# Kernel tuning notes

Measured on AMD Instinct MI355X. Metric: run time of the kernel, lower is better.

Reference implementation:

```python
import jax, jax.numpy as jnp
import numpy as np


def _vieta_pell_basis(x, degree):
    # Iterative recurrence: V0 = 2, V1 = x, Vn = x*V_{n-1} + V_{n-2}
    basis = [2.0 * jnp.ones_like(x), x]
    for _ in range(2, degree + 1):
        basis.append(x * basis[-1] + basis[-2])
    return jnp.stack(basis[: degree + 1], axis=-1)  # [b, i, d+1]


def setup_inputs() -> dict:
    key = jax.random.key(0)
    k1, k2 = jax.random.split(key)
    batch, input_dim, output_dim, degree = 4096, 1024, 1024, 8
    x = jax.random.normal(k1, (batch, input_dim), dtype=jnp.float32)
    std = 1.0 / (input_dim * (degree + 1))
    vp_coeffs = jax.random.normal(k2, (input_dim, output_dim, degree + 1), dtype=jnp.float32) * std
    return {"x": x, "vp_coeffs": vp_coeffs}


def reference(x, vp_coeffs):
    degree = vp_coeffs.shape[-1] - 1
    xt = jnp.tanh(x)  # [b, i]
    vp_basis = _vieta_pell_basis(xt, degree)  # [b, i, d+1]
    y = jnp.einsum("bid,iod->bo", vp_basis, vp_coeffs)
    return y
```

## Files before the change

kernel.cpp:

```cpp
#include <hip/hip_runtime.h>
#include <hip/hip_bf16.h>

typedef unsigned short u16;
typedef unsigned int   u32;

#define BATCH 4096
#define IDIM  1024
#define ODIM  1024
#define NDEG  9
#define KTOT  (IDIM * NDEG)

#define BM 128
#define BN 128
#define BKK 64

typedef __attribute__((ext_vector_type(8))) short short8_t;
typedef __attribute__((ext_vector_type(4))) float f32x4;

__device__ __forceinline__ u16 f2bf(float f) {
    union { float f; u32 u; } v; v.f = f;
    u32 r = v.u + 0x7FFFu + ((v.u >> 16) & 1u);
    return (u16)(r >> 16);
}
__device__ __forceinline__ u32 pack2bf(float lo, float hi) {
    return (u32)f2bf(lo) | ((u32)f2bf(hi) << 16);
}

__device__ __forceinline__ void gl_lds16(const u16* g, u16* l) {
    __builtin_amdgcn_global_load_lds(
        (const __attribute__((address_space(1))) void*)g,
        (__attribute__((address_space(3))) void*)l,
        16, 0, 0);
}

__global__ void prep_a_kernel(const float* __restrict__ x, u16* __restrict__ A) {
    int t  = blockIdx.x * 256 + threadIdx.x;
    int b  = t >> 9;
    int i2 = (t & 511) << 1;
    float2 xv = ((const float2*)x)[t];
    float t0 = tanhf(xv.x), t1 = tanhf(xv.y);
    u32* dst = (u32*)(A + (size_t)b * KTOT + i2);
    float a0 = 2.0f, a1 = 2.0f;
    float b0 = t0,  b1 = t1;
    dst[0]   = pack2bf(2.0f, 2.0f);
    dst[512] = pack2bf(t0, t1);
#pragma unroll
    for (int d = 2; d < NDEG; ++d) {
        float n0 = t0 * b0 + a0;
        float n1 = t1 * b1 + a1;
        dst[(size_t)d * 512] = pack2bf(n0, n1);
        a0 = b0; b0 = n0; a1 = b1; b1 = n1;
    }
}

__global__ void prep_b_kernel(const float* __restrict__ c, u16* __restrict__ Bt) {
    int t = blockIdx.x * 256 + threadIdx.x;
    int o = t >> 10;
    int i = t & 1023;
    const float* src = c + ((size_t)i * ODIM + o) * NDEG;
    u16* dst = Bt + (size_t)o * KTOT + i;
#pragma unroll
    for (int d = 0; d < NDEG; ++d)
        dst[(size_t)d * 1024] = f2bf(src[d]);
}

__global__ __launch_bounds__(256, 2)
void gemm_kernel(const u16* __restrict__ A, const u16* __restrict__ B,
                 float* __restrict__ C, int kLen) {
    __shared__ __align__(16) u16 ldsA[BM * BKK];
    __shared__ __align__(16) u16 ldsB[BN * BKK];

    const int tid  = threadIdx.x;
    const int lane = tid & 63;
    const int wave = tid >> 6;
    const int quad = lane >> 4;
    const int l15  = lane & 15;
    const int wm   = wave & 1;
    const int wn   = wave >> 1;
    const int bm   = blockIdx.y;
    const int bn   = blockIdx.x;
    const int kStart = blockIdx.z * kLen;
    C += (size_t)blockIdx.z * BATCH * ODIM;

    const u16* ga[4]; const u16* gb[4];
    u16* la[4]; u16* lb[4];
#pragma unroll
    for (int t = 0; t < 4; ++t) {
        int s  = t * 256 + tid;
        int r  = s >> 3;
        int sc = (s & 7) ^ (r & 7);
        ga[t] = A + (size_t)(bm * BM + r) * KTOT + kStart + sc * 8;
        gb[t] = B + (size_t)(bn * BN + r) * KTOT + kStart + sc * 8;
        la[t] = ldsA + s * 8;
        lb[t] = ldsB + s * 8;
    }

    f32x4 acc[4][4];
#pragma unroll
    for (int mt = 0; mt < 4; ++mt)
#pragma unroll
        for (int nt = 0; nt < 4; ++nt)
            acc[mt][nt] = (f32x4){0.f, 0.f, 0.f, 0.f};

    const int nIter = kLen / BKK;
    for (int it = 0; it < nIter; ++it) {
#pragma unroll
        for (int t = 0; t < 4; ++t) gl_lds16(ga[t], la[t]);
#pragma unroll
        for (int t = 0; t < 4; ++t) gl_lds16(gb[t], lb[t]);
        __syncthreads();

#pragma unroll
        for (int kk = 0; kk < 2; ++kk) {
            short8_t af[4], bfg[4];
#pragma unroll
            for (int mt = 0; mt < 4; ++mt) {
                int row = wm * 64 + mt * 16 + l15;
                int pc  = (kk * 4 + quad) ^ (row & 7);
                af[mt] = *(const short8_t*)(ldsA + (row * 8 + pc) * 8);
            }
#pragma unroll
            for (int nt = 0; nt < 4; ++nt) {
                int row = wn * 64 + nt * 16 + l15;
                int pc  = (kk * 4 + quad) ^ (row & 7);
                bfg[nt] = *(const short8_t*)(ldsB + (row * 8 + pc) * 8);
            }
#pragma unroll
            for (int mt = 0; mt < 4; ++mt)
#pragma unroll
                for (int nt = 0; nt < 4; ++nt)
                    acc[mt][nt] = __builtin_amdgcn_mfma_f32_16x16x32_bf16(
                        af[mt], bfg[nt], acc[mt][nt], 0, 0, 0);
        }
        __syncthreads();

#pragma unroll
        for (int t = 0; t < 4; ++t) { ga[t] += BKK; gb[t] += BKK; }
    }

#pragma unroll
    for (int mt = 0; mt < 4; ++mt) {
#pragma unroll
        for (int nt = 0; nt < 4; ++nt) {
            int row0 = bm * BM + wm * 64 + mt * 16 + quad * 4;
            int col  = bn * BN + wn * 64 + nt * 16 + l15;
#pragma unroll
            for (int r = 0; r < 4; ++r)
                C[(size_t)(row0 + r) * ODIM + col] = acc[mt][nt][r];
        }
    }
}

__global__ void reduce_kernel(const float* __restrict__ P, float* __restrict__ out) {
    int t = blockIdx.x * 256 + threadIdx.x;
    f32x4 a = ((const f32x4*)P)[t];
    f32x4 b = ((const f32x4*)(P + (size_t)BATCH * ODIM))[t];
    ((f32x4*)out)[t] = a + b;
}

extern "C" void kernel_launch(void* const* d_in, const int* in_sizes, int n_in,
                              void* d_out, int out_size, void* d_ws, size_t ws_size,
                              hipStream_t stream) {
    const float* x      = (const float*)d_in[0];
    const float* coeffs = (const float*)d_in[1];
    float* out = (float*)d_out;

    u16* A  = (u16*)d_ws;
    u16* Bt = A + (size_t)BATCH * KTOT;
    float* P = (float*)(Bt + (size_t)ODIM * KTOT);

    size_t need_base  = ((size_t)BATCH * KTOT + (size_t)ODIM * KTOT) * 2;
    size_t need_split = need_base + (size_t)2 * BATCH * ODIM * 4;

    prep_a_kernel<<<BATCH * IDIM / 512, 256, 0, stream>>>(x, A);
    prep_b_kernel<<<ODIM * IDIM / 256, 256, 0, stream>>>(coeffs, Bt);

    if (ws_size >= need_split) {
        dim3 grid(ODIM / BN, BATCH / BM, 2);
        gemm_kernel<<<grid, 256, 0, stream>>>(A, Bt, P, KTOT / 2);
        reduce_kernel<<<BATCH * ODIM / 1024, 256, 0, stream>>>(P, out);
    } else {
        dim3 grid(ODIM / BN, BATCH / BM, 1);
        gemm_kernel<<<grid, 256, 0, stream>>>(A, Bt, out, KTOT);
    }
}
```

Before: 220.1 us.

## Transpose coefficients through LDS tiles and raise split-K to four partitions

The coefficient prep kernel now stages a 128x72 tile in shared memory, so global reads are contiguous and writes to the transposed bf16 matrix are 8-byte vectors, replacing strided scalar accesses. The GEMM split-K factor goes from 2 to 4 when workspace allows, which gives more blocks to fill the CUs, and launch bounds ask for 4 blocks per CU. The reduce kernel becomes generic over S. The cost is more partial-sum traffic and a larger reduce, and the higher occupancy hint may cause register spills.

```diff
diff --git a/kernel.cpp b/kernel.cpp
--- a/kernel.cpp
+++ b/kernel.cpp
@@ -3,6 +3,7 @@
 
 typedef unsigned short u16;
 typedef unsigned int   u32;
+typedef unsigned long long u64;
 
 #define BATCH 4096
 #define IDIM  1024
@@ -53,18 +54,41 @@
     }
 }
 
+#define PB_TI 128
+#define PB_TO 8
+#define PB_J  (PB_TO * NDEG)
+#define PB_LS 132
+
 __global__ void prep_b_kernel(const float* __restrict__ c, u16* __restrict__ Bt) {
-    int t = blockIdx.x * 256 + threadIdx.x;
-    int o = t >> 10;
-    int i = t & 1023;
-    const float* src = c + ((size_t)i * ODIM + o) * NDEG;
-    u16* dst = Bt + (size_t)o * KTOT + i;
-#pragma unroll
-    for (int d = 0; d < NDEG; ++d)
-        dst[(size_t)d * 1024] = f2bf(src[d]);
-}
-
-__global__ __launch_bounds__(256, 2)
+    __shared__ u16 lds[PB_J * PB_LS];
+    const int tid = threadIdx.x;
+    const int i0  = blockIdx.y * PB_TI;
+    const int o0  = blockIdx.x * PB_TO;
+    const float* src = c + (size_t)i0 * (ODIM * NDEG) + (size_t)o0 * NDEG;
+
+#pragma unroll
+    for (int t = 0; t < 36; ++t) {
+        int f  = t * 256 + tid;
+        int ii = f / PB_J;
+        int j  = f - ii * PB_J;
+        float v = src[(size_t)ii * (ODIM * NDEG) + j];
+        lds[j * PB_LS + ii] = f2bf(v);
+    }
+    __syncthreads();
+
+#pragma unroll
+    for (int t = 0; t < 9; ++t) {
+        int g   = t * 256 + tid;
+        int j   = g >> 5;
+        int ii4 = (g & 31) << 2;
+        int o   = j / NDEG;
+        int d   = j - o * NDEG;
+        u64 v = *(const u64*)(lds + j * PB_LS + ii4);
+        *(u64*)(Bt + (size_t)(o0 + o) * KTOT + d * 1024 + i0 + ii4) = v;
+    }
+}
+
+__global__ __launch_bounds__(256, 4)
 void gemm_kernel(const u16* __restrict__ A, const u16* __restrict__ B,
                  float* __restrict__ C, int kLen) {
     __shared__ __align__(16) u16 ldsA[BM * BKK];
@@ -151,11 +175,13 @@
     }
 }
 
-__global__ void reduce_kernel(const float* __restrict__ P, float* __restrict__ out) {
+__global__ void reduce_kernel(const float* __restrict__ P, float* __restrict__ out,
+                              int S) {
     int t = blockIdx.x * 256 + threadIdx.x;
     f32x4 a = ((const f32x4*)P)[t];
-    f32x4 b = ((const f32x4*)(P + (size_t)BATCH * ODIM))[t];
-    ((f32x4*)out)[t] = a + b;
+    for (int s = 1; s < S; ++s)
+        a += ((const f32x4*)(P + (size_t)s * BATCH * ODIM))[t];
+    ((f32x4*)out)[t] = a;
 }
 
 extern "C" void kernel_launch(void* const* d_in, const int* in_sizes, int n_in,
@@ -169,16 +195,23 @@
     u16* Bt = A + (size_t)BATCH * KTOT;
     float* P = (float*)(Bt + (size_t)ODIM * KTOT);
 
-    size_t need_base  = ((size_t)BATCH * KTOT + (size_t)ODIM * KTOT) * 2;
-    size_t need_split = need_base + (size_t)2 * BATCH * ODIM * 4;
+    size_t need_base = ((size_t)BATCH * KTOT + (size_t)ODIM * KTOT) * 2;
+    size_t per_part  = (size_t)BATCH * ODIM * 4;
 
     prep_a_kernel<<<BATCH * IDIM / 512, 256, 0, stream>>>(x, A);
-    prep_b_kernel<<<ODIM * IDIM / 256, 256, 0, stream>>>(coeffs, Bt);
-
-    if (ws_size >= need_split) {
-        dim3 grid(ODIM / BN, BATCH / BM, 2);
-        gemm_kernel<<<grid, 256, 0, stream>>>(A, Bt, P, KTOT / 2);
-        reduce_kernel<<<BATCH * ODIM / 1024, 256, 0, stream>>>(P, out);
+    {
+        dim3 g(ODIM / PB_TO, IDIM / PB_TI);
+        prep_b_kernel<<<g, 256, 0, stream>>>(coeffs, Bt);
+    }
+
+    int S = 1;
+    if (ws_size >= need_base + 4 * per_part) S = 4;
+    else if (ws_size >= need_base + 2 * per_part) S = 2;
+
+    if (S > 1) {
+        dim3 grid(ODIM / BN, BATCH / BM, S);
+        gemm_kernel<<<grid, 256, 0, stream>>>(A, Bt, P, KTOT / S);
+        reduce_kernel<<<BATCH * ODIM / 1024, 256, 0, stream>>>(P, out, S);
     } else {
         dim3 grid(ODIM / BN, BATCH / BM, 1);
         gemm_kernel<<<grid, 256, 0, stream>>>(A, Bt, out, KTOT);
```

New measurement: 220.8 us. Within noise of the previous version (+0.3%).
